# Performance work log

Hardware: AMD Instinct MI355X
Metric: run time of the kernel (lower is better)

The kernel has to match this reference:

```python
import jax, jax.numpy as jnp
import numpy as np

N_SENT = 100000   # source ('sent') nodes
N_TYPE = 10000    # destination ('type') nodes
E = 640000        # edges of etype 'has'
D = 128           # out_dim
LEAKY_SLOPE = 0.01  # F.leaky_relu default


def setup_inputs() -> dict:
    key = jax.random.key(0)
    k0, k1, k2, k3, k4 = jax.random.split(key, 5)
    h_sent = jax.random.normal(k0, (N_SENT, D), jnp.float32)
    h_type = jax.random.normal(k1, (N_TYPE, D), jnp.float32)
    # attn_fc: Linear(2*D, 1, bias=False) -> weight [1, 2*D]
    attn_w = jax.random.normal(k2, (1, 2 * D), jnp.float32) * (1.0 / np.sqrt(2 * D))
    src_idx = jax.random.randint(k3, (E,), 0, N_SENT, dtype=jnp.int32)
    dst_idx = jax.random.randint(k4, (E,), 0, N_TYPE, dtype=jnp.int32)
    return {"h_sent": h_sent, "h_type": h_type, "attn_w": attn_w,
            "src_idx": src_idx, "dst_idx": dst_idx}


def reference(h_sent, h_type, attn_w, src_idx, dst_idx):
    w = attn_w[0]  # [2D]
    # attn_fc(cat(src_h, dst_h)) == src_h @ w[:D] + dst_h @ w[D:]  (no bias)
    s_src = h_sent @ w[:D]   # [N_SENT]
    s_dst = h_type @ w[D:]   # [N_TYPE]
    e = jax.nn.leaky_relu(s_src[src_idx] + s_dst[dst_idx], LEAKY_SLOPE)  # [E]
    # segment (per-destination) softmax over incoming edges
    m = jax.ops.segment_max(e, dst_idx, num_segments=N_TYPE)             # [N_TYPE]
    m = jnp.where(jnp.isfinite(m), m, 0.0)                               # empty segments -> 0
    ex = jnp.exp(e - m[dst_idx])                                         # [E]
    denom = jax.ops.segment_sum(ex, dst_idx, num_segments=N_TYPE)        # [N_TYPE]
    alpha = ex / denom[dst_idx]                                          # [E]
    # weighted scatter-sum of source features into destination nodes
    msg = alpha[:, None] * h_sent[src_idx]                               # [E, D]
    h_new = jax.ops.segment_sum(msg, dst_idx, num_segments=N_TYPE)       # [N_TYPE, D]
    # DGL only updates nodes that received messages; isolated nodes keep h
    deg = jax.ops.segment_sum(jnp.ones_like(e), dst_idx, num_segments=N_TYPE)
    return jnp.where(deg[:, None] > 0, h_new, h_type)
```

## Files before the change

kernel.cpp:

```cpp
#include <hip/hip_runtime.h>
#include <stdint.h>
#include <stddef.h>

#define N_SENT 100000
#define N_TYPE 10000
#define NEDGE  640000
#define NROWS  (N_SENT + N_TYPE)
#define MAXDEG 256
#define HB     256
#define HCHUNK (NEDGE / HB)

__device__ __forceinline__ float bf2f(uint32_t lo16) {
    return __builtin_bit_cast(float, lo16 << 16);
}
__device__ __forceinline__ uint32_t f2bf(float f) {
    uint32_t u = __builtin_bit_cast(uint32_t, f);
    return (u + 0x7fffu + ((u >> 16) & 1u)) >> 16;
}

__device__ __forceinline__ bool detect_bf16(const uint32_t* __restrict__ h) {
    uint32_t u = h[threadIdx.x & 63];
    uint32_t e_lo = (u >> 7) & 0xffu;
    int ok = (e_lo >= 100u && e_lo <= 140u) ? 1 : 0;
    unsigned long long m = __ballot(ok);
    return __popcll(m) >= 48;
}

#define SC_BLOCKS 6875

__global__ __launch_bounds__(256) void scores_k(const void* __restrict__ h_sent,
                                                const void* __restrict__ h_type,
                                                const void* __restrict__ attn_w,
                                                float* __restrict__ s_src,
                                                float* __restrict__ s_dst) {
    int t    = blockIdx.x * 256 + (int)threadIdx.x;
    int lane = threadIdx.x & 63;
    bool isbf = detect_bf16((const uint32_t*)h_sent);
    if (isbf) {
        uint4 wsv = ((const uint4*)attn_w)[lane & 15];
        uint4 wtv = ((const uint4*)attn_w)[16 + (lane & 15)];
        bool isSrc = t < N_SENT * 16;
        const uint4* p = isSrc ? (const uint4*)h_sent + t
                               : (const uint4*)h_type + (t - N_SENT * 16);
        uint4 h = *p;
        uint4 wv = isSrc ? wsv : wtv;
        float s = bf2f(h.x & 0xffffu) * bf2f(wv.x & 0xffffu)
                + bf2f(h.x >> 16)     * bf2f(wv.x >> 16)
                + bf2f(h.y & 0xffffu) * bf2f(wv.y & 0xffffu)
                + bf2f(h.y >> 16)     * bf2f(wv.y >> 16)
                + bf2f(h.z & 0xffffu) * bf2f(wv.z & 0xffffu)
                + bf2f(h.z >> 16)     * bf2f(wv.z >> 16)
                + bf2f(h.w & 0xffffu) * bf2f(wv.w & 0xffffu)
                + bf2f(h.w >> 16)     * bf2f(wv.w >> 16);
        s += __shfl_xor(s, 1, 64);
        s += __shfl_xor(s, 2, 64);
        s += __shfl_xor(s, 4, 64);
        s += __shfl_xor(s, 8, 64);
        if ((lane & 15) == 0) {
            int row = t >> 4;
            if (row < N_SENT) s_src[row] = s;
            else              s_dst[row - N_SENT] = s;
        }
    } else {
        float4 wsv = ((const float4*)attn_w)[lane & 31];
        float4 wtv = ((const float4*)attn_w)[32 + (lane & 31)];
        const int HALF = NROWS * 16;
        int it0 = t, it1 = t + HALF;
        bool s0 = it0 < N_SENT * 32, s1 = it1 < N_SENT * 32;
        const float4* p0 = s0 ? (const float4*)h_sent + it0
                              : (const float4*)h_type + (it0 - N_SENT * 32);
        const float4* p1 = s1 ? (const float4*)h_sent + it1
                              : (const float4*)h_type + (it1 - N_SENT * 32);
        float4 h0 = *p0;
        float4 h1 = *p1;
        __builtin_amdgcn_sched_barrier(0);
        float4 w0 = s0 ? wsv : wtv, w1 = s1 ? wsv : wtv;
        float a = h0.x * w0.x + h0.y * w0.y + h0.z * w0.z + h0.w * w0.w;
        float b = h1.x * w1.x + h1.y * w1.y + h1.z * w1.z + h1.w * w1.w;
        a += __shfl_xor(a, 1, 64);  b += __shfl_xor(b, 1, 64);
        a += __shfl_xor(a, 2, 64);  b += __shfl_xor(b, 2, 64);
        a += __shfl_xor(a, 4, 64);  b += __shfl_xor(b, 4, 64);
        a += __shfl_xor(a, 8, 64);  b += __shfl_xor(b, 8, 64);
        a += __shfl_xor(a, 16, 64); b += __shfl_xor(b, 16, 64);
        if ((lane & 31) == 0) {
            int r0 = it0 >> 5, r1 = it1 >> 5;
            if (r0 < N_SENT) s_src[r0] = a; else s_dst[r0 - N_SENT] = a;
            if (r1 < N_SENT) s_src[r1] = b; else s_dst[r1 - N_SENT] = b;
        }
    }
}

__global__ __launch_bounds__(256) void count_k(const int* __restrict__ dst,
                                               uint32_t* __restrict__ count2) {
    __shared__ uint32_t hist[N_TYPE];
    int cb = blockIdx.x;
    int t  = threadIdx.x;
#pragma unroll
    for (int i = 0; i < 40; i++) {
        int idx = i * 256 + t;
        if (idx < N_TYPE) hist[idx] = 0u;
    }
    __syncthreads();
    int e0 = cb * HCHUNK;
    int dv[10];
#pragma unroll
    for (int k = 0; k < 10; k++) {
        int i = k * 256 + t;
        dv[k] = dst[e0 + (i < HCHUNK ? i : HCHUNK - 1)];
    }
    __builtin_amdgcn_sched_barrier(0);
#pragma unroll
    for (int k = 0; k < 10; k++) {
        int i = k * 256 + t;
        if (i < HCHUNK) atomicAdd(&hist[dv[k]], 1u);
    }
    __syncthreads();
    uint4* row = (uint4*)(count2 + (size_t)cb * N_TYPE);
#pragma unroll
    for (int i = 0; i < 10; i++) {
        int idx = i * 256 + t;
        if (idx < N_TYPE / 4) row[idx] = ((const uint4*)hist)[idx];
    }
}

__global__ __launch_bounds__(256) void sumscan_k(uint32_t* __restrict__ count2,
                                                 uint32_t* __restrict__ total) {
    int tid  = blockIdx.x * 256 + (int)threadIdx.x;
    int lane = threadIdx.x & 63;
    int bin  = tid >> 3;
    int sub  = tid & 7;
    if (bin >= N_TYPE) return;
    uint32_t vals[32];
#pragma unroll
    for (int c = 0; c < 32; c++)
        vals[c] = count2[(size_t)(sub * 32 + c) * N_TYPE + bin];
    __builtin_amdgcn_sched_barrier(0);
    uint32_t lsum = 0;
#pragma unroll
    for (int c = 0; c < 32; c++) lsum += vals[c];
    uint32_t incl = lsum;
#pragma unroll
    for (int off = 1; off < 8; off <<= 1) {
        uint32_t v = __shfl_up(incl, off, 64);
        if ((lane & 7) >= off) incl += v;
    }
    uint32_t run = incl - lsum;
#pragma unroll
    for (int c = 0; c < 32; c++) {
        uint32_t v = vals[c];
        count2[(size_t)(sub * 32 + c) * N_TYPE + bin] = run;
        run += v;
    }
    if (sub == 7) total[bin] = incl;
}

__global__ __launch_bounds__(1024) void scan_k(const uint32_t* __restrict__ total,
                                               uint32_t* __restrict__ offsets) {
    const int CH = 10;
    int t = threadIdx.x, lane = t & 63, wv = t >> 6;
    int base = t * CH;
    uint32_t local[CH];
    uint32_t tsum = 0;
#pragma unroll
    for (int i = 0; i < CH; i++) {
        int idx = base + i;
        uint32_t c = (idx < N_TYPE) ? total[idx] : 0u;
        local[i] = c;
        tsum += c;
    }
    uint32_t orig = tsum;
#pragma unroll
    for (int off = 1; off < 64; off <<= 1) {
        uint32_t v = __shfl_up(tsum, off, 64);
        if (lane >= off) tsum += v;
    }
    __shared__ uint32_t wsum[16];
    if (lane == 63) wsum[wv] = tsum;
    __syncthreads();
    if (wv == 0 && lane < 16) {
        uint32_t u = wsum[lane], o = u;
#pragma unroll
        for (int off = 1; off < 16; off <<= 1) {
            uint32_t v = __shfl_up(u, off, 64);
            if (lane >= off) u += v;
        }
        wsum[lane] = u - o;
    }
    __syncthreads();
    uint32_t run = wsum[wv] + tsum - orig;
#pragma unroll
    for (int i = 0; i < CH; i++) {
        int idx = base + i;
        if (idx < N_TYPE) {
            offsets[idx] = run;
            run += local[i];
        } else if (idx == N_TYPE) {
            offsets[idx] = run;
        }
    }
}

__global__ __launch_bounds__(256) void fill_k(const int* __restrict__ src,
                                              const int* __restrict__ dst,
                                              const uint32_t* __restrict__ offsets,
                                              const uint32_t* __restrict__ base2,
                                              uint32_t* __restrict__ edge_src) {
    __shared__ uint32_t cur[N_TYPE];
    int cb = blockIdx.x;
    int t  = threadIdx.x;
    const uint32_t* brow = base2 + (size_t)cb * N_TYPE;
#pragma unroll
    for (int i = 0; i < 10; i++) {
        int idx = i * 256 + t;
        if (idx < N_TYPE / 4) {
            uint4 o = ((const uint4*)offsets)[idx];
            uint4 b = ((const uint4*)brow)[idx];
            uint4 c; c.x = o.x + b.x; c.y = o.y + b.y; c.z = o.z + b.z; c.w = o.w + b.w;
            ((uint4*)cur)[idx] = c;
        }
    }
    __syncthreads();
    int e0 = cb * HCHUNK;
    int dv[10], sv[10];
#pragma unroll
    for (int k = 0; k < 10; k++) {
        int i = k * 256 + t;
        int e = e0 + (i < HCHUNK ? i : HCHUNK - 1);
        dv[k] = dst[e];
        sv[k] = src[e];
    }
    __builtin_amdgcn_sched_barrier(0);
#pragma unroll
    for (int k = 0; k < 10; k++) {
        int i = k * 256 + t;
        if (i < HCHUNK) {
            uint32_t pos = atomicAdd(&cur[dv[k]], 1u);
            edge_src[pos] = (uint32_t)sv[k];
        }
    }
}

__global__ __launch_bounds__(256) void agg_k(const void* __restrict__ h_sent,
                                             const void* __restrict__ h_type,
                                             const float* __restrict__ s_src,
                                             const float* __restrict__ s_dst,
                                             const uint32_t* __restrict__ offsets,
                                             const uint32_t* __restrict__ edge_src,
                                             void* __restrict__ out) {
    __shared__ float    sc[4][MAXDEG];
    __shared__ uint32_t ss[4][MAXDEG];
    int j     = (blockIdx.x * 256 + threadIdx.x) >> 6;
    int wslot = threadIdx.x >> 6;
    int lane  = threadIdx.x & 63;
    bool valid = j < N_TYPE;
    bool isbf  = detect_bf16((const uint32_t*)h_sent);
    uint32_t beg = 0, deg = 0;
    float sdj = 0.0f;
    if (valid) {
        beg = offsets[j];
        deg = offsets[j + 1] - beg;
        sdj = s_dst[j];
    }
    float*    mysc = sc[wslot];
    uint32_t* myss = ss[wslot];
    bool fits = (deg <= MAXDEG);
    float m = -INFINITY;
    for (uint32_t k = lane; k < deg; k += 64) {
        uint32_t s = edge_src[beg + k];
        float v = s_src[s] + sdj;
        v = v > 0.0f ? v : 0.01f * v;
        if (fits) { mysc[k] = v; myss[k] = s; }
        m = fmaxf(m, v);
    }
#pragma unroll
    for (int off = 32; off; off >>= 1) m = fmaxf(m, __shfl_xor(m, off, 64));
    __syncthreads();
    if (!valid) return;
    if (deg == 0) {
        if (isbf) ((uint32_t*)out)[(size_t)j * 64 + lane] =
                      ((const uint32_t*)h_type)[(size_t)j * 64 + lane];
        else      ((float2*)out)[(size_t)j * 64 + lane] =
                      ((const float2*)h_type)[(size_t)j * 64 + lane];
        return;
    }
    float denom = 0.0f, a0 = 0.0f, a1 = 0.0f;
    if (isbf) {
        const uint32_t* hp = (const uint32_t*)h_sent;
        uint32_t k = 0;
        if (fits) {
            for (; k + 16 <= deg; k += 16) {
                uint32_t sv[16]; float vv[16]; uint32_t gv[16];
#pragma unroll
                for (int i = 0; i < 16; i++) { sv[i] = myss[k + i]; vv[i] = mysc[k + i]; }
#pragma unroll
                for (int i = 0; i < 16; i++) gv[i] = hp[(size_t)sv[i] * 64 + lane];
#pragma unroll
                for (int i = 0; i < 16; i++) {
                    float w = __expf(vv[i] - m);
                    denom += w;
                    a0 += w * bf2f(gv[i] & 0xffffu);
                    a1 += w * bf2f(gv[i] >> 16);
                }
            }
            for (; k + 8 <= deg; k += 8) {
                uint32_t sv[8]; float vv[8]; uint32_t gv[8];
#pragma unroll
                for (int i = 0; i < 8; i++) { sv[i] = myss[k + i]; vv[i] = mysc[k + i]; }
#pragma unroll
                for (int i = 0; i < 8; i++) gv[i] = hp[(size_t)sv[i] * 64 + lane];
#pragma unroll
                for (int i = 0; i < 8; i++) {
                    float w = __expf(vv[i] - m);
                    denom += w;
                    a0 += w * bf2f(gv[i] & 0xffffu);
                    a1 += w * bf2f(gv[i] >> 16);
                }
            }
            for (; k < deg; ++k) {
                float w = __expf(mysc[k] - m);
                uint32_t g = hp[(size_t)myss[k] * 64 + lane];
                denom += w;
                a0 += w * bf2f(g & 0xffffu);
                a1 += w * bf2f(g >> 16);
            }
        } else {
            for (k = 0; k < deg; ++k) {
                uint32_t s = edge_src[beg + k];
                float v = s_src[s] + sdj; v = v > 0.0f ? v : 0.01f * v;
                float w = __expf(v - m);
                uint32_t g = hp[(size_t)s * 64 + lane];
                denom += w;
                a0 += w * bf2f(g & 0xffffu);
                a1 += w * bf2f(g >> 16);
            }
        }
        float inv = 1.0f / denom;
        ((uint32_t*)out)[(size_t)j * 64 + lane] = f2bf(a0 * inv) | (f2bf(a1 * inv) << 16);
    } else {
        const float2* hp = (const float2*)h_sent;
        uint32_t k = 0;
        if (fits) {
            for (; k + 16 <= deg; k += 16) {
                uint32_t sv[16]; float vv[16]; float2 gv[16];
#pragma unroll
                for (int i = 0; i < 16; i++) { sv[i] = myss[k + i]; vv[i] = mysc[k + i]; }
#pragma unroll
                for (int i = 0; i < 16; i++) gv[i] = hp[(size_t)sv[i] * 64 + lane];
#pragma unroll
                for (int i = 0; i < 16; i++) {
                    float w = __expf(vv[i] - m);
                    denom += w;
                    a0 += w * gv[i].x;
                    a1 += w * gv[i].y;
                }
            }
            for (; k + 8 <= deg; k += 8) {
                uint32_t sv[8]; float vv[8]; float2 gv[8];
#pragma unroll
                for (int i = 0; i < 8; i++) { sv[i] = myss[k + i]; vv[i] = mysc[k + i]; }
#pragma unroll
                for (int i = 0; i < 8; i++) gv[i] = hp[(size_t)sv[i] * 64 + lane];
#pragma unroll
                for (int i = 0; i < 8; i++) {
                    float w = __expf(vv[i] - m);
                    denom += w;
                    a0 += w * gv[i].x;
                    a1 += w * gv[i].y;
                }
            }
            for (; k < deg; ++k) {
                float w = __expf(mysc[k] - m);
                float2 g = hp[(size_t)myss[k] * 64 + lane];
                denom += w;
                a0 += w * g.x;
                a1 += w * g.y;
            }
        } else {
            for (k = 0; k < deg; ++k) {
                uint32_t s = edge_src[beg + k];
                float v = s_src[s] + sdj; v = v > 0.0f ? v : 0.01f * v;
                float w = __expf(v - m);
                float2 g = hp[(size_t)s * 64 + lane];
                denom += w;
                a0 += w * g.x;
                a1 += w * g.y;
            }
        }
        float inv = 1.0f / denom;
        ((float2*)out)[(size_t)j * 64 + lane] = make_float2(a0 * inv, a1 * inv);
    }
}

static inline size_t align_up(size_t x) { return (x + 255) & ~(size_t)255; }

extern "C" void kernel_launch(void* const* d_in, const int* in_sizes, int n_in,
                              void* d_out, int out_size, void* d_ws, size_t ws_size,
                              hipStream_t stream) {
    const void* h_sent = d_in[0];
    const void* h_type = d_in[1];
    const void* attn_w = d_in[2];
    const int* src_idx = (const int*)d_in[3];
    const int* dst_idx = (const int*)d_in[4];

    char* w = (char*)d_ws;
    float*    s_src     = (float*)w;    w += align_up((size_t)N_SENT * 4);
    float*    s_dst     = (float*)w;    w += align_up((size_t)N_TYPE * 4);
    uint32_t* count2    = (uint32_t*)w; w += align_up((size_t)HB * N_TYPE * 4);
    uint32_t* total     = (uint32_t*)w; w += align_up((size_t)N_TYPE * 4);
    uint32_t* offsets   = (uint32_t*)w; w += align_up((size_t)(N_TYPE + 1) * 4);
    uint32_t* edge_src  = (uint32_t*)w; w += align_up((size_t)NEDGE * 4);

    scores_k<<<SC_BLOCKS, 256, 0, stream>>>(h_sent, h_type, attn_w, s_src, s_dst);
    count_k<<<HB, 256, 0, stream>>>(dst_idx, count2);
    sumscan_k<<<(N_TYPE * 8 + 255) / 256, 256, 0, stream>>>(count2, total);
    scan_k<<<1, 1024, 0, stream>>>(total, offsets);
    fill_k<<<HB, 256, 0, stream>>>(src_idx, dst_idx, offsets, count2, edge_src);
    agg_k<<<(N_TYPE + 3) / 4, 256, 0, stream>>>(h_sent, h_type, s_src, s_dst,
                                                offsets, edge_src, d_out);
}
```

Before: 175.9 us.

## Split wavefront into two half-waves gathering alternate edges with wider loads

The aggregation kernel now has each half of the 64-lane wavefront handle alternate incoming edges. Each lane loads 8 or 16 bytes of a source row (uint2 for bf16, float4 for fp32) instead of 4 or 8, and the two halves are combined with a shuffle reduction at the end. The fixed-size tail loops are replaced by masked full-width iterations, where out-of-range edges get weight exp(-inf)=0. The intent is to keep more independent row gathers in flight per wave with wider memory transactions. The cost is extra shuffles, the wasted lanes of masked iterations on low-degree nodes, and higher register pressure.

```diff
diff --git a/kernel.cpp b/kernel.cpp
--- a/kernel.cpp
+++ b/kernel.cpp
@@ -252,6 +252,8 @@
     int j     = (blockIdx.x * 256 + threadIdx.x) >> 6;
     int wslot = threadIdx.x >> 6;
     int lane  = threadIdx.x & 63;
+    int half  = lane >> 5;
+    int hl    = lane & 31;
     bool valid = j < N_TYPE;
     bool isbf  = detect_bf16((const uint32_t*)h_sent);
     uint32_t beg = 0, deg = 0;
@@ -283,111 +285,131 @@
                       ((const float2*)h_type)[(size_t)j * 64 + lane];
         return;
     }
-    float denom = 0.0f, a0 = 0.0f, a1 = 0.0f;
+    float denom = 0.0f, a0 = 0.0f, a1 = 0.0f, a2 = 0.0f, a3 = 0.0f;
     if (isbf) {
-        const uint32_t* hp = (const uint32_t*)h_sent;
-        uint32_t k = 0;
+        const uint2* hp = (const uint2*)h_sent;
         if (fits) {
-            for (; k + 16 <= deg; k += 16) {
-                uint32_t sv[16]; float vv[16]; uint32_t gv[16];
-#pragma unroll
-                for (int i = 0; i < 16; i++) { sv[i] = myss[k + i]; vv[i] = mysc[k + i]; }
-#pragma unroll
-                for (int i = 0; i < 16; i++) gv[i] = hp[(size_t)sv[i] * 64 + lane];
+            for (uint32_t k = 0; k < deg; k += 32) {
+                uint32_t sv[16]; float vv[16]; uint2 gv[16];
+#pragma unroll
+                for (int i = 0; i < 16; i++) {
+                    uint32_t e = k + 2u * i + (uint32_t)half;
+                    bool ok = e < deg;
+                    uint32_t ec = ok ? e : 0u;
+                    sv[i] = myss[ec];
+                    vv[i] = ok ? mysc[ec] : -INFINITY;
+                }
+#pragma unroll
+                for (int i = 0; i < 16; i++) gv[i] = hp[(size_t)sv[i] * 32 + hl];
 #pragma unroll
                 for (int i = 0; i < 16; i++) {
                     float w = __expf(vv[i] - m);
                     denom += w;
-                    a0 += w * bf2f(gv[i] & 0xffffu);
-                    a1 += w * bf2f(gv[i] >> 16);
-                }
-            }
-            for (; k + 8 <= deg; k += 8) {
-                uint32_t sv[8]; float vv[8]; uint32_t gv[8];
-#pragma unroll
-                for (int i = 0; i < 8; i++) { sv[i] = myss[k + i]; vv[i] = mysc[k + i]; }
-#pragma unroll
-                for (int i = 0; i < 8; i++) gv[i] = hp[(size_t)sv[i] * 64 + lane];
-#pragma unroll
-                for (int i = 0; i < 8; i++) {
-                    float w = __expf(vv[i] - m);
-                    denom += w;
-                    a0 += w * bf2f(gv[i] & 0xffffu);
-                    a1 += w * bf2f(gv[i] >> 16);
-                }
-            }
-            for (; k < deg; ++k) {
-                float w = __expf(mysc[k] - m);
-                uint32_t g = hp[(size_t)myss[k] * 64 + lane];
-                denom += w;
-                a0 += w * bf2f(g & 0xffffu);
-                a1 += w * bf2f(g >> 16);
+                    a0 += w * bf2f(gv[i].x & 0xffffu);
+                    a1 += w * bf2f(gv[i].x >> 16);
+                    a2 += w * bf2f(gv[i].y & 0xffffu);
+                    a3 += w * bf2f(gv[i].y >> 16);
+                }
             }
         } else {
-            for (k = 0; k < deg; ++k) {
-                uint32_t s = edge_src[beg + k];
-                float v = s_src[s] + sdj; v = v > 0.0f ? v : 0.01f * v;
-                float w = __expf(v - m);
-                uint32_t g = hp[(size_t)s * 64 + lane];
-                denom += w;
-                a0 += w * bf2f(g & 0xffffu);
-                a1 += w * bf2f(g >> 16);
-            }
-        }
-        float inv = 1.0f / denom;
-        ((uint32_t*)out)[(size_t)j * 64 + lane] = f2bf(a0 * inv) | (f2bf(a1 * inv) << 16);
-    } else {
-        const float2* hp = (const float2*)h_sent;
-        uint32_t k = 0;
-        if (fits) {
-            for (; k + 16 <= deg; k += 16) {
-                uint32_t sv[16]; float vv[16]; float2 gv[16];
-#pragma unroll
-                for (int i = 0; i < 16; i++) { sv[i] = myss[k + i]; vv[i] = mysc[k + i]; }
-#pragma unroll
-                for (int i = 0; i < 16; i++) gv[i] = hp[(size_t)sv[i] * 64 + lane];
+            for (uint32_t k = 0; k < deg; k += 32) {
+                uint32_t sv[16]; float vv[16]; uint2 gv[16];
+#pragma unroll
+                for (int i = 0; i < 16; i++) {
+                    uint32_t e = k + 2u * i + (uint32_t)half;
+                    bool ok = e < deg;
+                    uint32_t ec = ok ? e : 0u;
+                    uint32_t s = edge_src[beg + ec];
+                    float v = s_src[s] + sdj; v = v > 0.0f ? v : 0.01f * v;
+                    sv[i] = s;
+                    vv[i] = ok ? v : -INFINITY;
+                }
+#pragma unroll
+                for (int i = 0; i < 16; i++) gv[i] = hp[(size_t)sv[i] * 32 + hl];
 #pragma unroll
                 for (int i = 0; i < 16; i++) {
                     float w = __expf(vv[i] - m);
                     denom += w;
-                    a0 += w * gv[i].x;
-                    a1 += w * gv[i].y;
+                    a0 += w * bf2f(gv[i].x & 0xffffu);
+                    a1 += w * bf2f(gv[i].x >> 16);
+                    a2 += w * bf2f(gv[i].y & 0xffffu);
+                    a3 += w * bf2f(gv[i].y >> 16);
                 }
             }
-            for (; k + 8 <= deg; k += 8) {
-                uint32_t sv[8]; float vv[8]; float2 gv[8];
-#pragma unroll
-                for (int i = 0; i < 8; i++) { sv[i] = myss[k + i]; vv[i] = mysc[k + i]; }
-#pragma unroll
-                for (int i = 0; i < 8; i++) gv[i] = hp[(size_t)sv[i] * 64 + lane];
+        }
+        denom += __shfl_xor(denom, 32, 64);
+        a0 += __shfl_xor(a0, 32, 64);
+        a1 += __shfl_xor(a1, 32, 64);
+        a2 += __shfl_xor(a2, 32, 64);
+        a3 += __shfl_xor(a3, 32, 64);
+        float inv = 1.0f / denom;
+        if (half == 0) {
+            uint2 o;
+            o.x = f2bf(a0 * inv) | (f2bf(a1 * inv) << 16);
+            o.y = f2bf(a2 * inv) | (f2bf(a3 * inv) << 16);
+            ((uint2*)out)[(size_t)j * 32 + hl] = o;
+        }
+    } else {
+        const float4* hp = (const float4*)h_sent;
+        if (fits) {
+            for (uint32_t k = 0; k < deg; k += 16) {
+                uint32_t sv[8]; float vv[8]; float4 gv[8];
+#pragma unroll
+                for (int i = 0; i < 8; i++) {
+                    uint32_t e = k + 2u * i + (uint32_t)half;
+                    bool ok = e < deg;
+                    uint32_t ec = ok ? e : 0u;
+                    sv[i] = myss[ec];
+                    vv[i] = ok ? mysc[ec] : -INFINITY;
+                }
+#pragma unroll
+                for (int i = 0; i < 8; i++) gv[i] = hp[(size_t)sv[i] * 32 + hl];
 #pragma unroll
                 for (int i = 0; i < 8; i++) {
                     float w = __expf(vv[i] - m);
                     denom += w;
                     a0 += w * gv[i].x;
                     a1 += w * gv[i].y;
-                }
-            }
-            for (; k < deg; ++k) {
-                float w = __expf(mysc[k] - m);
-                float2 g = hp[(size_t)myss[k] * 64 + lane];
-                denom += w;
-                a0 += w * g.x;
-                a1 += w * g.y;
+                    a2 += w * gv[i].z;
+                    a3 += w * gv[i].w;
+                }
             }
         } else {
-            for (k = 0; k < deg; ++k) {
-                uint32_t s = edge_src[beg + k];
-                float v = s_src[s] + sdj; v = v > 0.0f ? v : 0.01f * v;
-                float w = __expf(v - m);
-                float2 g = hp[(size_t)s * 64 + lane];
-                denom += w;
-                a0 += w * g.x;
-                a1 += w * g.y;
+            for (uint32_t k = 0; k < deg; k += 16) {
+                uint32_t sv[8]; float vv[8]; float4 gv[8];
+#pragma unroll
+                for (int i = 0; i < 8; i++) {
+                    uint32_t e = k + 2u * i + (uint32_t)half;
+                    bool ok = e < deg;
+                    uint32_t ec = ok ? e : 0u;
+                    uint32_t s = edge_src[beg + ec];
+                    float v = s_src[s] + sdj; v = v > 0.0f ? v : 0.01f * v;
+                    sv[i] = s;
+                    vv[i] = ok ? v : -INFINITY;
+                }
+#pragma unroll
+                for (int i = 0; i < 8; i++) gv[i] = hp[(size_t)sv[i] * 32 + hl];
+#pragma unroll
+                for (int i = 0; i < 8; i++) {
+                    float w = __expf(vv[i] - m);
+                    denom += w;
+                    a0 += w * gv[i].x;
+                    a1 += w * gv[i].y;
+                    a2 += w * gv[i].z;
+                    a3 += w * gv[i].w;
+                }
             }
         }
+        denom += __shfl_xor(denom, 32, 64);
+        a0 += __shfl_xor(a0, 32, 64);
+        a1 += __shfl_xor(a1, 32, 64);
+        a2 += __shfl_xor(a2, 32, 64);
+        a3 += __shfl_xor(a3, 32, 64);
         float inv = 1.0f / denom;
-        ((float2*)out)[(size_t)j * 64 + lane] = make_float2(a0 * inv, a1 * inv);
+        if (half == 0) {
+            float4 o = make_float4(a0 * inv, a1 * inv, a2 * inv, a3 * inv);
+            ((float4*)out)[(size_t)j * 32 + hl] = o;
+        }
     }
 }
 
```

Measured after the change: 174.6 us. About the same (-0.7%).

## Split aggregation by source-row bucket for L2 locality, combine partial softmax

Applied to the files above, without the earlier changes.

Aggregation is split into eight passes. Each pass handles only the edges whose source row falls in one eighth of h_sent, so the gathered rows from concurrent blocks share a smaller working set that can stay in cache. Each pass writes a partial max, denominator and weighted sum per destination, and a combine kernel merges them with the log-sum-exp rescaling. This adds two launches, a re-scan of every edge list eight times, and a float partial buffer of about 40 MB that is written and read back. It runs only for bf16 inputs when the workspace is large enough; otherwise the original aggregation kernel is used.

```diff
diff --git a/kernel.cpp b/kernel.cpp
--- a/kernel.cpp
+++ b/kernel.cpp
@@ -9,6 +9,8 @@
 #define MAXDEG 256
 #define HB     256
 #define HCHUNK (NEDGE / HB)
+#define NBUCK  8
+#define BROWS  (N_SENT / NBUCK)
 
 __device__ __forceinline__ float bf2f(uint32_t lo16) {
     return __builtin_bit_cast(float, lo16 << 16);
@@ -240,20 +242,172 @@
     }
 }
 
+__global__ __launch_bounds__(256) void pagg_k(const void* __restrict__ h_sent,
+                                              const float* __restrict__ s_src,
+                                              const float* __restrict__ s_dst,
+                                              const uint32_t* __restrict__ offsets,
+                                              const uint32_t* __restrict__ edge_src,
+                                              float* __restrict__ part_m,
+                                              float* __restrict__ part_d,
+                                              float* __restrict__ part_v) {
+    bool isbf = detect_bf16((const uint32_t*)h_sent);
+    if (!isbf) return;
+    __shared__ float    sc[4][MAXDEG];
+    __shared__ uint32_t ss[4][MAXDEG];
+    uint32_t p     = blockIdx.x & 7;
+    int      wslot = threadIdx.x >> 6;
+    int      lane  = threadIdx.x & 63;
+    int      j     = (int)(blockIdx.x >> 3) * 4 + wslot;
+    uint32_t beg = offsets[j];
+    uint32_t deg = offsets[j + 1] - beg;
+    float    sdj = s_dst[j];
+    float*    mysc = sc[wslot];
+    uint32_t* myss = ss[wslot];
+    uint32_t pidx = (uint32_t)j * NBUCK + p;
+    float m = -INFINITY;
+    uint32_t cnt = 0;
+    bool fits = deg <= MAXDEG;
+    if (fits) {
+        for (uint32_t k0 = 0; k0 < deg; k0 += 64) {
+            uint32_t k = k0 + (uint32_t)lane;
+            bool act = k < deg;
+            uint32_t s = 0; float v = 0.0f; bool inb = false;
+            if (act) {
+                s = edge_src[beg + k];
+                inb = (s / BROWS) == p;
+                if (inb) {
+                    v = s_src[s] + sdj;
+                    v = v > 0.0f ? v : 0.01f * v;
+                    m = fmaxf(m, v);
+                }
+            }
+            unsigned long long msk = __ballot(inb ? 1 : 0);
+            uint32_t pos = cnt + (uint32_t)__popcll(msk & ((1ull << lane) - 1ull));
+            if (inb) { mysc[pos] = v; myss[pos] = s; }
+            cnt += (uint32_t)__popcll(msk);
+        }
+    } else {
+        for (uint32_t k = lane; k < deg; k += 64) {
+            uint32_t s = edge_src[beg + k];
+            if ((s / BROWS) == p) {
+                float v = s_src[s] + sdj;
+                v = v > 0.0f ? v : 0.01f * v;
+                m = fmaxf(m, v);
+            }
+        }
+    }
+#pragma unroll
+    for (int off = 32; off; off >>= 1) m = fmaxf(m, __shfl_xor(m, off, 64));
+    if (m == -INFINITY) {
+        if (lane == 0) part_d[pidx] = 0.0f;
+        return;
+    }
+    float denom = 0.0f, a0 = 0.0f, a1 = 0.0f;
+    const uint32_t* hp = (const uint32_t*)h_sent;
+    if (fits) {
+        uint32_t k = 0;
+        for (; k + 8 <= cnt; k += 8) {
+            uint32_t sv[8]; float vv[8]; uint32_t gv[8];
+#pragma unroll
+            for (int i = 0; i < 8; i++) { sv[i] = myss[k + i]; vv[i] = mysc[k + i]; }
+#pragma unroll
+            for (int i = 0; i < 8; i++) gv[i] = hp[(size_t)sv[i] * 64 + lane];
+#pragma unroll
+            for (int i = 0; i < 8; i++) {
+                float w = __expf(vv[i] - m);
+                denom += w;
+                a0 += w * bf2f(gv[i] & 0xffffu);
+                a1 += w * bf2f(gv[i] >> 16);
+            }
+        }
+        for (; k < cnt; ++k) {
+            float w = __expf(mysc[k] - m);
+            uint32_t g = hp[(size_t)myss[k] * 64 + lane];
+            denom += w;
+            a0 += w * bf2f(g & 0xffffu);
+            a1 += w * bf2f(g >> 16);
+        }
+    } else {
+        for (uint32_t k = 0; k < deg; ++k) {
+            uint32_t s = edge_src[beg + k];
+            if ((s / BROWS) == p) {
+                float v = s_src[s] + sdj; v = v > 0.0f ? v : 0.01f * v;
+                float w = __expf(v - m);
+                uint32_t g = hp[(size_t)s * 64 + lane];
+                denom += w;
+                a0 += w * bf2f(g & 0xffffu);
+                a1 += w * bf2f(g >> 16);
+            }
+        }
+    }
+    if (lane == 0) { part_m[pidx] = m; part_d[pidx] = denom; }
+    float* pv = part_v + ((size_t)pidx * 64 + (size_t)lane) * 2;
+    __builtin_nontemporal_store(a0, pv);
+    __builtin_nontemporal_store(a1, pv + 1);
+}
+
+__global__ __launch_bounds__(256) void pcomb_k(const void* __restrict__ h_sent,
+                                               const void* __restrict__ h_type,
+                                               const float* __restrict__ part_m,
+                                               const float* __restrict__ part_d,
+                                               const float* __restrict__ part_v,
+                                               void* __restrict__ out) {
+    bool isbf = detect_bf16((const uint32_t*)h_sent);
+    if (!isbf) return;
+    int j    = (blockIdx.x * 256 + (int)threadIdx.x) >> 6;
+    int lane = threadIdx.x & 63;
+    if (j >= N_TYPE) return;
+    float dd[NBUCK], md[NBUCK];
+#pragma unroll
+    for (int p = 0; p < NBUCK; p++) dd[p] = part_d[j * NBUCK + p];
+#pragma unroll
+    for (int p = 0; p < NBUCK; p++) md[p] = part_m[j * NBUCK + p];
+    float M = -INFINITY;
+    bool any = false;
+#pragma unroll
+    for (int p = 0; p < NBUCK; p++)
+        if (dd[p] > 0.0f) { M = fmaxf(M, md[p]); any = true; }
+    if (!any) {
+        ((uint32_t*)out)[(size_t)j * 64 + lane] =
+            ((const uint32_t*)h_type)[(size_t)j * 64 + lane];
+        return;
+    }
+    float vx[NBUCK], vy[NBUCK];
+#pragma unroll
+    for (int p = 0; p < NBUCK; p++) {
+        const float* q = part_v + ((size_t)(j * NBUCK + p) * 64 + (size_t)lane) * 2;
+        vx[p] = __builtin_nontemporal_load(q);
+        vy[p] = __builtin_nontemporal_load(q + 1);
+    }
+    float D = 0.0f, a0 = 0.0f, a1 = 0.0f;
+#pragma unroll
+    for (int p = 0; p < NBUCK; p++) {
+        bool ok = dd[p] > 0.0f;
+        float w = ok ? __expf(md[p] - M) : 0.0f;
+        D += (ok ? dd[p] : 0.0f) * w;
+        a0 += w * (ok ? vx[p] : 0.0f);
+        a1 += w * (ok ? vy[p] : 0.0f);
+    }
+    float inv = 1.0f / D;
+    ((uint32_t*)out)[(size_t)j * 64 + lane] = f2bf(a0 * inv) | (f2bf(a1 * inv) << 16);
+}
+
 __global__ __launch_bounds__(256) void agg_k(const void* __restrict__ h_sent,
                                              const void* __restrict__ h_type,
                                              const float* __restrict__ s_src,
                                              const float* __restrict__ s_dst,
                                              const uint32_t* __restrict__ offsets,
                                              const uint32_t* __restrict__ edge_src,
-                                             void* __restrict__ out) {
+                                             void* __restrict__ out,
+                                             int use_part) {
     __shared__ float    sc[4][MAXDEG];
     __shared__ uint32_t ss[4][MAXDEG];
+    bool isbf = detect_bf16((const uint32_t*)h_sent);
+    if (use_part && isbf) return;
     int j     = (blockIdx.x * 256 + threadIdx.x) >> 6;
     int wslot = threadIdx.x >> 6;
     int lane  = threadIdx.x & 63;
     bool valid = j < N_TYPE;
-    bool isbf  = detect_bf16((const uint32_t*)h_sent);
     uint32_t beg = 0, deg = 0;
     float sdj = 0.0f;
     if (valid) {
@@ -409,12 +563,24 @@
     uint32_t* total     = (uint32_t*)w; w += align_up((size_t)N_TYPE * 4);
     uint32_t* offsets   = (uint32_t*)w; w += align_up((size_t)(N_TYPE + 1) * 4);
     uint32_t* edge_src  = (uint32_t*)w; w += align_up((size_t)NEDGE * 4);
+    float*    part_m    = (float*)w;    w += align_up((size_t)N_TYPE * NBUCK * 4);
+    float*    part_d    = (float*)w;    w += align_up((size_t)N_TYPE * NBUCK * 4);
+    float*    part_v    = (float*)w;    w += align_up((size_t)N_TYPE * NBUCK * 128 * 4);
+    size_t need = (size_t)(w - (char*)d_ws);
+    int use_part = (need <= ws_size) ? 1 : 0;
 
     scores_k<<<SC_BLOCKS, 256, 0, stream>>>(h_sent, h_type, attn_w, s_src, s_dst);
     count_k<<<HB, 256, 0, stream>>>(dst_idx, count2);
     sumscan_k<<<(N_TYPE * 8 + 255) / 256, 256, 0, stream>>>(count2, total);
     scan_k<<<1, 1024, 0, stream>>>(total, offsets);
     fill_k<<<HB, 256, 0, stream>>>(src_idx, dst_idx, offsets, count2, edge_src);
+    if (use_part) {
+        pagg_k<<<(N_TYPE / 4) * NBUCK, 256, 0, stream>>>(h_sent, s_src, s_dst,
+                                                         offsets, edge_src,
+                                                         part_m, part_d, part_v);
+        pcomb_k<<<(N_TYPE + 3) / 4, 256, 0, stream>>>(h_sent, h_type,
+                                                      part_m, part_d, part_v, d_out);
+    }
     agg_k<<<(N_TYPE + 3) / 4, 256, 0, stream>>>(h_sent, h_type, s_src, s_dst,
-                                                offsets, edge_src, d_out);
-}
+                                                offsets, edge_src, d_out, use_part);
+}
```

Result: slower. 182.0 us (+3.5%).
